# Kernel optimization log

Hardware: AMD Instinct MI355X
Metric: run time of the kernel (lower is better)

## Reference

```python
import jax, jax.numpy as jnp
import numpy as np

SOFT_BLEND = 20.0
INIT_BONES = np.array([0, 1, 2, 4, 5, 16, 17, 18, 19])
MAX_STEPS = 20
CVG_THRESH = 1e-5
DVG_THRESH = 1.0
EPS = 1e-6


def mlp(x, W0, b0, W1, b1, W2, b2):
    h = jax.nn.softplus(x @ W0 + b0)
    h = jax.nn.softplus(h @ W1 + b1)
    return h @ W2 + b2


def query_weights(x, params):
    # lbs_network -> soft_blend * logits -> softmax  (softmax_mode='softmax')
    return jax.nn.softmax(SOFT_BLEND * mlp(x, *params), axis=-1)


def forward_skinning(xc, params, tfs):
    # xc [B,N,3], tfs [B,J,4,4] -> xd [B,N,3]  (LBS: blend transforms with weights)
    w = query_weights(xc, params)                                    # [B,N,J]
    xh = jnp.concatenate([xc, jnp.ones_like(xc[..., :1])], -1)       # [B,N,4]
    return jnp.einsum('bpn,bnij,bpj->bpi', w, tfs, xh)[..., :3]


def gradient(xc, params, tfs):
    # per-point jacobian d(forward_skinning)/d(xc): [B,N,3,3]
    def f(x, tfs_b):
        w = query_weights(x, params)                                 # [J]
        xh = jnp.concatenate([x, jnp.ones((1,), x.dtype)])
        return jnp.einsum('j,jik,k->i', w, tfs_b, xh)[:3]
    jac = jax.jacfwd(f)
    return jax.vmap(jax.vmap(jac, in_axes=(0, None)), in_axes=(0, 0))(xc, tfs)


def broyden(g, x_init, J_inv_init):
    # vectorized Broyden: the torch data-dependent boolean masking becomes
    # mask-gated jnp.where updates; the early break becomes a fixed-length scan
    # (iterations are no-ops once ids_val is all False).
    x = x_init                                                       # [M,3,1]
    J_inv = J_inv_init                                               # [M,3,3]
    gx = g(x)
    update = -(J_inv @ gx)
    gx_norm_opt = jnp.linalg.norm(gx[..., 0], axis=-1)               # [M]
    state = (x, gx, J_inv, update, gx_norm_opt,
             jnp.zeros_like(x), jnp.zeros_like(gx),
             jnp.ones_like(gx_norm_opt, dtype=bool))

    def step(s, _):
        x, gx, J_inv, update, gx_norm_opt, delta_x, delta_gx, ids_val = s
        m = ids_val[:, None, None]
        delta_x = jnp.where(m, update, delta_x)
        x = x + jnp.where(m, delta_x, 0.0)
        gx_new = g(x)
        delta_gx = jnp.where(m, gx_new - gx, delta_gx)
        gx = jnp.where(m, gx_new, gx)
        gx_norm = jnp.linalg.norm(gx[..., 0], axis=-1)
        ids_opt = gx_norm < gx_norm_opt
        gx_norm_opt = jnp.where(ids_opt, gx_norm, gx_norm_opt)
        ids_val = (gx_norm_opt > CVG_THRESH) & (gx_norm < DVG_THRESH)
        m2 = ids_val[:, None, None]
        vT = jnp.swapaxes(delta_x, -1, -2) @ J_inv                   # [M,1,3]
        a = delta_x - J_inv @ delta_gx                               # [M,3,1]
        b = vT @ delta_gx                                            # [M,1,1]
        b = b + jnp.where(b >= 0, EPS, -EPS)
        J_inv = J_inv + jnp.where(m2, (a / b) @ vT, 0.0)
        update = -(J_inv @ gx)
        return (x, gx, J_inv, update, gx_norm_opt, delta_x, delta_gx, ids_val), None

    state, _ = jax.lax.scan(step, state, None, length=MAX_STEPS)
    # in the torch code x_opt aliases x, so the returned root is the final x
    return state[0], state[4]


def _forward(xd, tfs, W0, b0, W1, b1, W2, b2):
    params = (W0, b0, W1, b1, W2, b2)
    sg = jax.lax.stop_gradient
    B, N, D = xd.shape
    I = len(INIT_BONES)
    # ---- init: inverse rigid transform per init bone (one-hot weights) ----
    xdh = jnp.concatenate([xd, jnp.ones_like(xd[..., :1])], -1)      # [B,N,4]
    T_inv = jnp.linalg.inv(tfs[:, INIT_BONES])                        # [B,I,4,4]
    xc_init = jnp.einsum('bcij,bnj->bnci', T_inv, xdh)[..., :3]       # [B,N,I,3]
    # ---- Broyden correspondence search (torch.no_grad) ----
    params_sg = tuple(sg(p) for p in params)
    tfs_sg = sg(tfs)
    xc_flat = sg(xc_init).reshape(B, N * I, D)
    xd_tgt = sg(jnp.repeat(xd, I, axis=1))                            # [B,N*I,3]
    J_inv_init = jnp.linalg.inv(gradient(xc_flat, params_sg, tfs_sg)).reshape(-1, D, D)

    def g(x):                                                         # [M,3,1] -> [M,3,1]
        xc = x[..., 0].reshape(B, N * I, D)
        err = forward_skinning(xc, params_sg, tfs_sg) - xd_tgt
        return err.reshape(-1, D, 1)

    x_opt, _ = broyden(g, xc_flat.reshape(-1, D, 1), J_inv_init)
    xc_opt = sg(x_opt[..., 0].reshape(B, N * I, D))
    # ---- implicit differentiation correction term ----
    xd_opt = forward_skinning(xc_opt, params, tfs)
    grad_inv = sg(jnp.linalg.inv(gradient(xc_opt, params, tfs)))      # [B,M,3,3]
    correction = xd_opt - sg(xd_opt)
    correction = jnp.einsum('bnij,bnj->bni', -grad_inv, correction)
    return (xc_opt + correction).reshape(B, N, I, D)


def setup_inputs():
    key = jax.random.key(0)
    ks = jax.random.split(key, 6)
    B, N, J, W = 1, 30000, 24, 64
    xd = 0.5 * jax.random.normal(ks[0], (B, N, 3), jnp.float32)
    # near-rigid bone transforms: identity + small perturbation, homogeneous last row
    R = jnp.eye(3, dtype=jnp.float32) + 0.1 * jax.random.normal(ks[1], (B, J, 3, 3), jnp.float32)
    t = 0.2 * jax.random.normal(ks[2], (B, J, 3, 1), jnp.float32)
    bot = jnp.broadcast_to(jnp.array([0., 0., 0., 1.], jnp.float32), (B, J, 1, 4))
    tfs = jnp.concatenate([jnp.concatenate([R, t], -1), bot], -2)     # [B,J,4,4]
    W0 = 0.5 * jax.random.normal(ks[3], (3, W), jnp.float32)
    W1 = jax.random.normal(ks[4], (W, W), jnp.float32) / float(np.sqrt(W))
    W2 = 0.1 * jax.random.normal(ks[5], (W, J), jnp.float32) / float(np.sqrt(W))
    return {"xd": xd, "tfs": tfs,
            "W0": W0, "b0": jnp.zeros((W,), jnp.float32),
            "W1": W1, "b1": jnp.zeros((W,), jnp.float32),
            "W2": W2, "b2": jnp.zeros((J,), jnp.float32)}


def reference(xd, tfs, W0, b0, W1, b1, W2, b2):
    return _forward(xd, tfs, W0, b0, W1, b1, W2, b2)
```

## Files before the change

### kernel.cpp

```cpp
#include <hip/hip_runtime.h>
#include <math.h>

#define TPB 64
#define NPT 270000
#define SOFTB 20.0f
#define CVGT 1e-5f
#define DVGT 1.0f
#define EPSB 1e-6f

#define WS_TINV 0
#define WS_W0T  256

typedef __attribute__((ext_vector_type(2))) float f2;

__device__ __forceinline__ f2 pk_fma(f2 a, f2 b, f2 c) {
#if __has_builtin(__builtin_elementwise_fma)
    return __builtin_elementwise_fma(a, b, c);
#else
    f2 r; r.x = fmaf(a.x, b.x, c.x); r.y = fmaf(a.y, b.y, c.y); return r;
#endif
}

__global__ void prep_kernel(const float* __restrict__ tfs,
                            const float* __restrict__ W0, const float* __restrict__ b0,
                            float* __restrict__ ws) {
    int t = threadIdx.x;
    if (t < 9) {
        const int bones[9] = {0, 1, 2, 4, 5, 16, 17, 18, 19};
        const float* T = tfs + bones[t] * 16;
        float r00=T[0], r01=T[1], r02=T[2],  t0=T[3];
        float r10=T[4], r11=T[5], r12=T[6],  t1=T[7];
        float r20=T[8], r21=T[9], r22=T[10], t2=T[11];
        float c00 = r11*r22 - r12*r21;
        float c01 = r12*r20 - r10*r22;
        float c02 = r10*r21 - r11*r20;
        float det = r00*c00 + r01*c01 + r02*c02;
        float id  = 1.0f / det;
        float i00=c00*id, i01=(r02*r21-r01*r22)*id, i02=(r01*r12-r02*r11)*id;
        float i10=c01*id, i11=(r00*r22-r02*r20)*id, i12=(r02*r10-r00*r12)*id;
        float i20=c02*id, i21=(r01*r20-r00*r21)*id, i22=(r00*r11-r01*r10)*id;
        float* O = ws + WS_TINV + t * 16;
        O[0]=i00; O[1]=i01; O[2]=i02;  O[3]=-(i00*t0+i01*t1+i02*t2);
        O[4]=i10; O[5]=i11; O[6]=i12;  O[7]=-(i10*t0+i11*t1+i12*t2);
        O[8]=i20; O[9]=i21; O[10]=i22; O[11]=-(i20*t0+i21*t1+i22*t2);
        O[12]=0.f; O[13]=0.f; O[14]=0.f; O[15]=1.f;
    }
    for (int i = t; i < 64*4; i += 256) {
        int k = i >> 2, cidx = i & 3;
        ws[WS_W0T + i] = (cidx < 3) ? W0[cidx*64 + k] : b0[k];
    }
}

__global__ __launch_bounds__(TPB) void deform_kernel(
    const float* __restrict__ xd,
    const float* __restrict__ tfs,
    const float* __restrict__ W1, const float* __restrict__ b1,
    const float* __restrict__ W2, const float* __restrict__ b2,
    const float* __restrict__ ws,
    float* __restrict__ out)
{
    __shared__ float stash[24 * TPB];

    const int tid = threadIdx.x;
    const int p   = blockIdx.x * TPB + tid;
    const bool live = (p < NPT);
    const int pc = live ? p : 0;
    const int n  = pc / 9;
    const int c  = pc - n * 9;

    float tx0 = xd[n*3+0], tx1 = xd[n*3+1], tx2 = xd[n*3+2];

    const float* Ti  = ws + WS_TINV + c * 16;
    const float* W0T = ws + WS_W0T;

    float x0 = fmaf(Ti[0], tx0, fmaf(Ti[1], tx1, fmaf(Ti[2],  tx2, Ti[3])));
    float x1 = fmaf(Ti[4], tx0, fmaf(Ti[5], tx1, fmaf(Ti[6],  tx2, Ti[7])));
    float x2 = fmaf(Ti[8], tx0, fmaf(Ti[9], tx1, fmaf(Ti[10], tx2, Ti[11])));

    f2 wr[12];

    auto forward = [&](float a0, float a1, float a2, float& o0, float& o1, float& o2) {
        const f2* b2v = (const f2*)b2;
        #pragma unroll
        for (int q = 0; q < 12; ++q) wr[q] = b2v[q];
        #pragma unroll 1
        for (int cc = 0; cc < 2; ++cc) {
            f2 z1[16];
            const f2* b1c = (const f2*)(b1 + cc*32);
            #pragma unroll
            for (int j = 0; j < 16; ++j) z1[j] = b1c[j];
            #pragma unroll 2
            for (int k = 0; k < 64; ++k) {
                float w0a = W0T[k*4+0], w0b = W0T[k*4+1], w0c = W0T[k*4+2], w0d = W0T[k*4+3];
                float z  = fmaf(a0, w0a, fmaf(a1, w0b, fmaf(a2, w0c, w0d)));
                float hk = fmaxf(z, 0.f) + __logf(1.f + __expf(-fabsf(z)));
                f2 hk2 = hk;
                const f2* Wr2 = (const f2*)(W1 + k*64 + cc*32);
                #pragma unroll
                for (int j = 0; j < 16; ++j) z1[j] = pk_fma(hk2, Wr2[j], z1[j]);
            }
            #pragma unroll
            for (int j = 0; j < 16; ++j) {
                float za = z1[j].x, zb = z1[j].y;
                float ha = fmaxf(za, 0.f) + __logf(1.f + __expf(-fabsf(za)));
                float hb = fmaxf(zb, 0.f) + __logf(1.f + __expf(-fabsf(zb)));
                const f2* Wa = (const f2*)(W2 + (cc*32 + 2*j  )*24);
                const f2* Wb = (const f2*)(W2 + (cc*32 + 2*j+1)*24);
                f2 ha2 = ha, hb2 = hb;
                #pragma unroll
                for (int q = 0; q < 12; ++q) wr[q] = pk_fma(ha2, Wa[q], wr[q]);
                #pragma unroll
                for (int q = 0; q < 12; ++q) wr[q] = pk_fma(hb2, Wb[q], wr[q]);
            }
        }
        f2 m0 = __builtin_elementwise_max(wr[0], wr[1]);
        f2 m1 = __builtin_elementwise_max(wr[2], wr[3]);
        f2 m2 = __builtin_elementwise_max(wr[4], wr[5]);
        f2 m3 = __builtin_elementwise_max(wr[6], wr[7]);
        f2 m4 = __builtin_elementwise_max(wr[8], wr[9]);
        f2 m5 = __builtin_elementwise_max(wr[10], wr[11]);
        m0 = __builtin_elementwise_max(m0, m1);
        m2 = __builtin_elementwise_max(m2, m3);
        m4 = __builtin_elementwise_max(m4, m5);
        m0 = __builtin_elementwise_max(m0, m2);
        m0 = __builtin_elementwise_max(m0, m4);
        float mx = fmaxf(m0.x, m0.y);
        float ssum = 0.f;
        #pragma unroll
        for (int q = 0; q < 12; ++q) {
            float ea = __expf(SOFTB*(wr[q].x - mx));
            float eb = __expf(SOFTB*(wr[q].y - mx));
            wr[q].x = ea; wr[q].y = eb;
            ssum += ea; ssum += eb;
        }
        float inv = 1.0f / ssum;
        o0 = 0.f; o1 = 0.f; o2 = 0.f;
        #pragma unroll
        for (int q = 0; q < 24; ++q) {
            float wq = ((q & 1) ? wr[q>>1].y : wr[q>>1].x) * inv;
            if (q & 1) wr[q>>1].y = wq; else wr[q>>1].x = wq;
            const float* Tn = tfs + q*16;
            float y0 = fmaf(Tn[0], a0, fmaf(Tn[1], a1, fmaf(Tn[2],  a2, Tn[3])));
            float y1 = fmaf(Tn[4], a0, fmaf(Tn[5], a1, fmaf(Tn[6],  a2, Tn[7])));
            float y2 = fmaf(Tn[8], a0, fmaf(Tn[9], a1, fmaf(Tn[10], a2, Tn[11])));
            o0 = fmaf(wq, y0, o0); o1 = fmaf(wq, y1, o1); o2 = fmaf(wq, y2, o2);
        }
    };

    float f0, f1, f2s;
    forward(x0, x1, x2, f0, f1, f2s);

    #pragma unroll
    for (int q = 0; q < 24; ++q)
        stash[q*TPB + tid] = (q & 1) ? wr[q>>1].y : wr[q>>1].x;

    float Jm[9];
    #pragma unroll 1
    for (int t = 0; t < 3; ++t) {
        float dot = 0.f, sA = 0.f, sB = 0.f, sC = 0.f;
        #pragma unroll 1
        for (int cc = 0; cc < 4; ++cc) {
            f2 z1c[8], d1c[8];
            const f2* b1c = (const f2*)(b1 + cc*16);
            #pragma unroll
            for (int j = 0; j < 8; ++j) { z1c[j] = b1c[j]; d1c[j] = (f2)0.f; }
            #pragma unroll 2
            for (int k = 0; k < 64; ++k) {
                float w0a = W0T[k*4+0], w0b = W0T[k*4+1], w0c = W0T[k*4+2], w0d = W0T[k*4+3];
                float wt  = W0T[k*4 + t];
                float z  = fmaf(x0, w0a, fmaf(x1, w0b, fmaf(x2, w0c, w0d)));
                float e  = __expf(-z);
                float hk = z + __logf(1.f + e);
                float sg = 1.0f / (1.0f + e);
                float dh0 = sg * wt;
                f2 hk2 = hk, dh02 = dh0;
                const f2* Wr2 = (const f2*)(W1 + k*64 + cc*16);
                #pragma unroll
                for (int j = 0; j < 8; ++j) {
                    z1c[j] = pk_fma(hk2,  Wr2[j], z1c[j]);
                    d1c[j] = pk_fma(dh02, Wr2[j], d1c[j]);
                }
            }
            f2 dmc[12];
            #pragma unroll
            for (int q = 0; q < 12; ++q) dmc[q] = (f2)0.f;
            #pragma unroll
            for (int j = 0; j < 16; ++j) {
                float zz = (j & 1) ? z1c[j>>1].y : z1c[j>>1].x;
                float dd = (j & 1) ? d1c[j>>1].y : d1c[j>>1].x;
                float sg1 = 1.0f / (1.0f + __expf(-zz));
                float dh1 = dd * sg1;
                f2 dh12 = dh1;
                const f2* W2r = (const f2*)(W2 + (cc*16 + j)*24);
                #pragma unroll
                for (int q = 0; q < 12; ++q) dmc[q] = pk_fma(dh12, W2r[q], dmc[q]);
            }
            #pragma unroll
            for (int q = 0; q < 24; ++q) {
                float dmq = (q & 1) ? dmc[q>>1].y : dmc[q>>1].x;
                float wd = stash[q*TPB + tid] * dmq;
                dot += wd;
                const float* Tn = tfs + q*16;
                float y0 = fmaf(Tn[0], x0, fmaf(Tn[1], x1, fmaf(Tn[2],  x2, Tn[3])));
                float y1 = fmaf(Tn[4], x0, fmaf(Tn[5], x1, fmaf(Tn[6],  x2, Tn[7])));
                float y2 = fmaf(Tn[8], x0, fmaf(Tn[9], x1, fmaf(Tn[10], x2, Tn[11])));
                sA = fmaf(wd, y0, sA); sB = fmaf(wd, y1, sB); sC = fmaf(wd, y2, sC);
            }
        }
        float ab0 = 0.f, ab1 = 0.f, ab2 = 0.f;
        #pragma unroll
        for (int q = 0; q < 24; ++q) {
            float wq = stash[q*TPB + tid];
            const float* Tn = tfs + q*16;
            ab0 = fmaf(wq, Tn[0 + t], ab0);
            ab1 = fmaf(wq, Tn[4 + t], ab1);
            ab2 = fmaf(wq, Tn[8 + t], ab2);
        }
        Jm[0 + t] = ab0 + SOFTB*(sA - dot*f0);
        Jm[3 + t] = ab1 + SOFTB*(sB - dot*f1);
        Jm[6 + t] = ab2 + SOFTB*(sC - dot*f2s);
    }

    {
        float m00=Jm[0], m01=Jm[1], m02=Jm[2];
        float m10=Jm[3], m11=Jm[4], m12=Jm[5];
        float m20=Jm[6], m21=Jm[7], m22=Jm[8];
        float c00 = m11*m22 - m12*m21, c01 = m12*m20 - m10*m22, c02 = m10*m21 - m11*m20;
        float det = m00*c00 + m01*c01 + m02*c02;
        float idet = 1.0f / det;
        stash[ 0*TPB+tid] = c00*idet;
        stash[ 1*TPB+tid] = (m02*m21-m01*m22)*idet;
        stash[ 2*TPB+tid] = (m01*m12-m02*m11)*idet;
        stash[ 3*TPB+tid] = c01*idet;
        stash[ 4*TPB+tid] = (m00*m22-m02*m20)*idet;
        stash[ 5*TPB+tid] = (m02*m10-m00*m12)*idet;
        stash[ 6*TPB+tid] = c02*idet;
        stash[ 7*TPB+tid] = (m01*m20-m00*m21)*idet;
        stash[ 8*TPB+tid] = (m00*m11-m01*m10)*idet;
    }
    stash[13*TPB+tid] = tx0;
    stash[14*TPB+tid] = tx1;
    stash[15*TPB+tid] = tx2;

    float g0 = f0 - tx0, g1 = f1 - tx1, g2 = f2s - tx2;
    float u0, u1, u2;
    {
        float Ji0=stash[0*TPB+tid], Ji1=stash[1*TPB+tid], Ji2=stash[2*TPB+tid];
        float Ji3=stash[3*TPB+tid], Ji4=stash[4*TPB+tid], Ji5=stash[5*TPB+tid];
        float Ji6=stash[6*TPB+tid], Ji7=stash[7*TPB+tid], Ji8=stash[8*TPB+tid];
        stash[9*TPB+tid] = sqrtf(g0*g0 + g1*g1 + g2*g2);
        u0 = -(Ji0*g0 + Ji1*g1 + Ji2*g2);
        u1 = -(Ji3*g0 + Ji4*g1 + Ji5*g2);
        u2 = -(Ji6*g0 + Ji7*g1 + Ji8*g2);
    }
    bool valid = true;

    for (int it = 0; it < 20; ++it) {
        if (!__any((int)valid)) break;
        if (valid) {
            stash[10*TPB+tid] = u0;
            stash[11*TPB+tid] = u1;
            stash[12*TPB+tid] = u2;
            x0 += u0; x1 += u1; x2 += u2;
            float fn0, fn1, fn2;
            forward(x0, x1, x2, fn0, fn1, fn2);
            float ng0 = fn0 - stash[13*TPB+tid];
            float ng1 = fn1 - stash[14*TPB+tid];
            float ng2 = fn2 - stash[15*TPB+tid];
            float dg0 = ng0 - g0, dg1 = ng1 - g1, dg2 = ng2 - g2;
            g0 = ng0; g1 = ng1; g2 = ng2;
            float gn  = sqrtf(g0*g0 + g1*g1 + g2*g2);
            float gno = fminf(gn, stash[9*TPB+tid]);
            stash[9*TPB+tid] = gno;
            valid = (gno > CVGT) && (gn < DVGT);
            if (valid) {
                float Ji0=stash[0*TPB+tid], Ji1=stash[1*TPB+tid], Ji2=stash[2*TPB+tid];
                float Ji3=stash[3*TPB+tid], Ji4=stash[4*TPB+tid], Ji5=stash[5*TPB+tid];
                float Ji6=stash[6*TPB+tid], Ji7=stash[7*TPB+tid], Ji8=stash[8*TPB+tid];
                float dx0=stash[10*TPB+tid], dx1=stash[11*TPB+tid], dx2=stash[12*TPB+tid];
                float v0 = dx0*Ji0 + dx1*Ji3 + dx2*Ji6;
                float v1 = dx0*Ji1 + dx1*Ji4 + dx2*Ji7;
                float v2 = dx0*Ji2 + dx1*Ji5 + dx2*Ji8;
                float a0 = dx0 - (Ji0*dg0 + Ji1*dg1 + Ji2*dg2);
                float a1 = dx1 - (Ji3*dg0 + Ji4*dg1 + Ji5*dg2);
                float a2 = dx2 - (Ji6*dg0 + Ji7*dg1 + Ji8*dg2);
                float b = v0*dg0 + v1*dg1 + v2*dg2;
                b += (b >= 0.f) ? EPSB : -EPSB;
                float ib = 1.0f / b;
                a0 *= ib; a1 *= ib; a2 *= ib;
                Ji0 = fmaf(a0, v0, Ji0); Ji1 = fmaf(a0, v1, Ji1); Ji2 = fmaf(a0, v2, Ji2);
                Ji3 = fmaf(a1, v0, Ji3); Ji4 = fmaf(a1, v1, Ji4); Ji5 = fmaf(a1, v2, Ji5);
                Ji6 = fmaf(a2, v0, Ji6); Ji7 = fmaf(a2, v1, Ji7); Ji8 = fmaf(a2, v2, Ji8);
                stash[0*TPB+tid]=Ji0; stash[1*TPB+tid]=Ji1; stash[2*TPB+tid]=Ji2;
                stash[3*TPB+tid]=Ji3; stash[4*TPB+tid]=Ji4; stash[5*TPB+tid]=Ji5;
                stash[6*TPB+tid]=Ji6; stash[7*TPB+tid]=Ji7; stash[8*TPB+tid]=Ji8;
                u0 = -(Ji0*g0 + Ji1*g1 + Ji2*g2);
                u1 = -(Ji3*g0 + Ji4*g1 + Ji5*g2);
                u2 = -(Ji6*g0 + Ji7*g1 + Ji8*g2);
            }
        }
    }

    if (live) {
        out[p*3+0] = x0;
        out[p*3+1] = x1;
        out[p*3+2] = x2;
    }
}

extern "C" void kernel_launch(void* const* d_in, const int* in_sizes, int n_in,
                              void* d_out, int out_size, void* d_ws, size_t ws_size,
                              hipStream_t stream) {
    const float* xd  = (const float*)d_in[0];
    const float* tfs = (const float*)d_in[1];
    const float* W0  = (const float*)d_in[2];
    const float* b0  = (const float*)d_in[3];
    const float* W1  = (const float*)d_in[4];
    const float* b1  = (const float*)d_in[5];
    const float* W2  = (const float*)d_in[6];
    const float* b2  = (const float*)d_in[7];
    float* out = (float*)d_out;
    float* ws  = (float*)d_ws;

    prep_kernel<<<1, 256, 0, stream>>>(tfs, W0, b0, ws);
    int nblk = (NPT + TPB - 1) / TPB;
    deform_kernel<<<nblk, TPB, 0, stream>>>(xd, tfs, W1, b1, W2, b2, ws, out);
}
```

Before: 798.4 us.

## Compute all three Jacobian columns in one pass over the MLP hidden layer

The Jacobian used to be built one input column at a time, and each pass recomputed the layer-0 softplus and the layer-1 pre-activations. It now runs a single loop over eight chunks of eight hidden units and carries three tangent accumulators (dA, dB, dC) beside z1, which cuts the repeated exp/log and W1 fma work roughly threefold. The diff also swaps exact divisions for the fast reciprocal intrinsic. The price is more live registers per thread, which could reduce occupancy or cause spills.

```diff
diff --git a/kernel.cpp b/kernel.cpp
--- a/kernel.cpp
+++ b/kernel.cpp
@@ -154,44 +154,52 @@
     for (int q = 0; q < 24; ++q)
         stash[q*TPB + tid] = (q & 1) ? wr[q>>1].y : wr[q>>1].x;
 
-    float Jm[9];
+    float dt0=0.f, dt1=0.f, dt2=0.f;
+    float sx0=0.f, sx1=0.f, sx2=0.f;
+    float sy0=0.f, sy1=0.f, sy2=0.f;
+    float sz0=0.f, sz1=0.f, sz2=0.f;
     #pragma unroll 1
-    for (int t = 0; t < 3; ++t) {
-        float dot = 0.f, sA = 0.f, sB = 0.f, sC = 0.f;
-        #pragma unroll 1
-        for (int cc = 0; cc < 4; ++cc) {
-            f2 z1c[8], d1c[8];
-            const f2* b1c = (const f2*)(b1 + cc*16);
-            #pragma unroll
-            for (int j = 0; j < 8; ++j) { z1c[j] = b1c[j]; d1c[j] = (f2)0.f; }
-            #pragma unroll 2
-            for (int k = 0; k < 64; ++k) {
-                float w0a = W0T[k*4+0], w0b = W0T[k*4+1], w0c = W0T[k*4+2], w0d = W0T[k*4+3];
-                float wt  = W0T[k*4 + t];
-                float z  = fmaf(x0, w0a, fmaf(x1, w0b, fmaf(x2, w0c, w0d)));
-                float e  = __expf(-z);
-                float hk = z + __logf(1.f + e);
-                float sg = 1.0f / (1.0f + e);
-                float dh0 = sg * wt;
-                f2 hk2 = hk, dh02 = dh0;
-                const f2* Wr2 = (const f2*)(W1 + k*64 + cc*16);
-                #pragma unroll
-                for (int j = 0; j < 8; ++j) {
-                    z1c[j] = pk_fma(hk2,  Wr2[j], z1c[j]);
-                    d1c[j] = pk_fma(dh02, Wr2[j], d1c[j]);
-                }
-            }
+    for (int cc = 0; cc < 8; ++cc) {
+        f2 z1c[4], dA[4], dB[4], dC[4];
+        const f2* b1c = (const f2*)(b1 + cc*8);
+        #pragma unroll
+        for (int j = 0; j < 4; ++j) {
+            z1c[j] = b1c[j]; dA[j] = (f2)0.f; dB[j] = (f2)0.f; dC[j] = (f2)0.f;
+        }
+        #pragma unroll 2
+        for (int k = 0; k < 64; ++k) {
+            float w0a = W0T[k*4+0], w0b = W0T[k*4+1], w0c = W0T[k*4+2], w0d = W0T[k*4+3];
+            float z  = fmaf(x0, w0a, fmaf(x1, w0b, fmaf(x2, w0c, w0d)));
+            float e  = __expf(-z);
+            float hk = z + __logf(1.f + e);
+            float sg = __builtin_amdgcn_rcpf(1.f + e);
+            float da = sg * w0a, db = sg * w0b, dc = sg * w0c;
+            f2 hk2 = hk, da2 = da, db2 = db, dc2 = dc;
+            const f2* Wr2 = (const f2*)(W1 + k*64 + cc*8);
+            #pragma unroll
+            for (int j = 0; j < 4; ++j) {
+                z1c[j] = pk_fma(hk2, Wr2[j], z1c[j]);
+                dA[j]  = pk_fma(da2, Wr2[j], dA[j]);
+                dB[j]  = pk_fma(db2, Wr2[j], dB[j]);
+                dC[j]  = pk_fma(dc2, Wr2[j], dC[j]);
+            }
+        }
+        float sg1[8];
+        #pragma unroll
+        for (int j = 0; j < 8; ++j) {
+            float zz = (j & 1) ? z1c[j>>1].y : z1c[j>>1].x;
+            sg1[j] = __builtin_amdgcn_rcpf(1.f + __expf(-zz));
+        }
+        auto do_t = [&](const f2* dX, float& dt, float& sx, float& sy, float& sz) {
             f2 dmc[12];
             #pragma unroll
             for (int q = 0; q < 12; ++q) dmc[q] = (f2)0.f;
             #pragma unroll
-            for (int j = 0; j < 16; ++j) {
-                float zz = (j & 1) ? z1c[j>>1].y : z1c[j>>1].x;
-                float dd = (j & 1) ? d1c[j>>1].y : d1c[j>>1].x;
-                float sg1 = 1.0f / (1.0f + __expf(-zz));
-                float dh1 = dd * sg1;
+            for (int j = 0; j < 8; ++j) {
+                float dd  = (j & 1) ? dX[j>>1].y : dX[j>>1].x;
+                float dh1 = dd * sg1[j];
                 f2 dh12 = dh1;
-                const f2* W2r = (const f2*)(W2 + (cc*16 + j)*24);
+                const f2* W2r = (const f2*)(W2 + (cc*8 + j)*24);
                 #pragma unroll
                 for (int q = 0; q < 12; ++q) dmc[q] = pk_fma(dh12, W2r[q], dmc[q]);
             }
@@ -199,32 +207,41 @@
             for (int q = 0; q < 24; ++q) {
                 float dmq = (q & 1) ? dmc[q>>1].y : dmc[q>>1].x;
                 float wd = stash[q*TPB + tid] * dmq;
-                dot += wd;
+                dt += wd;
                 const float* Tn = tfs + q*16;
                 float y0 = fmaf(Tn[0], x0, fmaf(Tn[1], x1, fmaf(Tn[2],  x2, Tn[3])));
                 float y1 = fmaf(Tn[4], x0, fmaf(Tn[5], x1, fmaf(Tn[6],  x2, Tn[7])));
                 float y2 = fmaf(Tn[8], x0, fmaf(Tn[9], x1, fmaf(Tn[10], x2, Tn[11])));
-                sA = fmaf(wd, y0, sA); sB = fmaf(wd, y1, sB); sC = fmaf(wd, y2, sC);
-            }
-        }
-        float ab0 = 0.f, ab1 = 0.f, ab2 = 0.f;
-        #pragma unroll
-        for (int q = 0; q < 24; ++q) {
-            float wq = stash[q*TPB + tid];
-            const float* Tn = tfs + q*16;
-            ab0 = fmaf(wq, Tn[0 + t], ab0);
-            ab1 = fmaf(wq, Tn[4 + t], ab1);
-            ab2 = fmaf(wq, Tn[8 + t], ab2);
-        }
-        Jm[0 + t] = ab0 + SOFTB*(sA - dot*f0);
-        Jm[3 + t] = ab1 + SOFTB*(sB - dot*f1);
-        Jm[6 + t] = ab2 + SOFTB*(sC - dot*f2s);
-    }
+                sx = fmaf(wd, y0, sx); sy = fmaf(wd, y1, sy); sz = fmaf(wd, y2, sz);
+            }
+        };
+        do_t(dA, dt0, sx0, sy0, sz0);
+        do_t(dB, dt1, sx1, sy1, sz1);
+        do_t(dC, dt2, sx2, sy2, sz2);
+    }
+
+    float ab00=0.f, ab01=0.f, ab02=0.f;
+    float ab10=0.f, ab11=0.f, ab12=0.f;
+    float ab20=0.f, ab21=0.f, ab22=0.f;
+    #pragma unroll
+    for (int q = 0; q < 24; ++q) {
+        float wq = stash[q*TPB + tid];
+        const float* Tn = tfs + q*16;
+        ab00 = fmaf(wq, Tn[0],  ab00); ab01 = fmaf(wq, Tn[1],  ab01); ab02 = fmaf(wq, Tn[2],  ab02);
+        ab10 = fmaf(wq, Tn[4],  ab10); ab11 = fmaf(wq, Tn[5],  ab11); ab12 = fmaf(wq, Tn[6],  ab12);
+        ab20 = fmaf(wq, Tn[8],  ab20); ab21 = fmaf(wq, Tn[9],  ab21); ab22 = fmaf(wq, Tn[10], ab22);
+    }
+    float m00 = ab00 + SOFTB*(sx0 - dt0*f0);
+    float m01 = ab01 + SOFTB*(sx1 - dt1*f0);
+    float m02 = ab02 + SOFTB*(sx2 - dt2*f0);
+    float m10 = ab10 + SOFTB*(sy0 - dt0*f1);
+    float m11 = ab11 + SOFTB*(sy1 - dt1*f1);
+    float m12 = ab12 + SOFTB*(sy2 - dt2*f1);
+    float m20 = ab20 + SOFTB*(sz0 - dt0*f2s);
+    float m21 = ab21 + SOFTB*(sz1 - dt1*f2s);
+    float m22 = ab22 + SOFTB*(sz2 - dt2*f2s);
 
     {
-        float m00=Jm[0], m01=Jm[1], m02=Jm[2];
-        float m10=Jm[3], m11=Jm[4], m12=Jm[5];
-        float m20=Jm[6], m21=Jm[7], m22=Jm[8];
         float c00 = m11*m22 - m12*m21, c01 = m12*m20 - m10*m22, c02 = m10*m21 - m11*m20;
         float det = m00*c00 + m01*c01 + m02*c02;
         float idet = 1.0f / det;
```

Measured after the change: 1.135 ms. 1.42x slower.

## Split each point across two threads by halving hidden layer-2 units

Applied to the files above, without the earlier changes.

Each point is now handled by a pair of adjacent lanes. Each lane computes half of the second hidden layer's units and its share of the output logits and jacobian contributions, then the pair combines partial sums with xor-shuffles. The launch uses twice as many threads, and only the even lane writes the result. This aims to cut per-thread serial FMA work and raise parallelism. In exchange, both lanes repeat the layer-1 softplus, the softmax, the bone transforms and the Broyden bookkeeping, and the change adds shuffle traffic.

```diff
diff --git a/kernel.cpp b/kernel.cpp
--- a/kernel.cpp
+++ b/kernel.cpp
@@ -62,7 +62,9 @@
     __shared__ float stash[24 * TPB];
 
     const int tid = threadIdx.x;
-    const int p   = blockIdx.x * TPB + tid;
+    const int gt  = blockIdx.x * TPB + tid;
+    const int p    = gt >> 1;
+    const int half = gt & 1;
     const bool live = (p < NPT);
     const int pc = live ? p : 0;
     const int n  = pc / 9;
@@ -82,36 +84,40 @@
     auto forward = [&](float a0, float a1, float a2, float& o0, float& o1, float& o2) {
         const f2* b2v = (const f2*)b2;
         #pragma unroll
-        for (int q = 0; q < 12; ++q) wr[q] = b2v[q];
-        #pragma unroll 1
-        for (int cc = 0; cc < 2; ++cc) {
-            f2 z1[16];
-            const f2* b1c = (const f2*)(b1 + cc*32);
-            #pragma unroll
-            for (int j = 0; j < 16; ++j) z1[j] = b1c[j];
-            #pragma unroll 2
-            for (int k = 0; k < 64; ++k) {
-                float w0a = W0T[k*4+0], w0b = W0T[k*4+1], w0c = W0T[k*4+2], w0d = W0T[k*4+3];
-                float z  = fmaf(a0, w0a, fmaf(a1, w0b, fmaf(a2, w0c, w0d)));
-                float hk = fmaxf(z, 0.f) + __logf(1.f + __expf(-fabsf(z)));
-                f2 hk2 = hk;
-                const f2* Wr2 = (const f2*)(W1 + k*64 + cc*32);
-                #pragma unroll
-                for (int j = 0; j < 16; ++j) z1[j] = pk_fma(hk2, Wr2[j], z1[j]);
-            }
-            #pragma unroll
-            for (int j = 0; j < 16; ++j) {
-                float za = z1[j].x, zb = z1[j].y;
-                float ha = fmaxf(za, 0.f) + __logf(1.f + __expf(-fabsf(za)));
-                float hb = fmaxf(zb, 0.f) + __logf(1.f + __expf(-fabsf(zb)));
-                const f2* Wa = (const f2*)(W2 + (cc*32 + 2*j  )*24);
-                const f2* Wb = (const f2*)(W2 + (cc*32 + 2*j+1)*24);
-                f2 ha2 = ha, hb2 = hb;
-                #pragma unroll
-                for (int q = 0; q < 12; ++q) wr[q] = pk_fma(ha2, Wa[q], wr[q]);
-                #pragma unroll
-                for (int q = 0; q < 12; ++q) wr[q] = pk_fma(hb2, Wb[q], wr[q]);
-            }
+        for (int q = 0; q < 12; ++q) wr[q] = half ? (f2)0.f : b2v[q];
+        f2 z1[16];
+        const f2* b1v = (const f2*)(b1 + half*32);
+        #pragma unroll
+        for (int j = 0; j < 16; ++j) z1[j] = b1v[j];
+        #pragma unroll 2
+        for (int k = 0; k < 64; ++k) {
+            float w0a = W0T[k*4+0], w0b = W0T[k*4+1], w0c = W0T[k*4+2], w0d = W0T[k*4+3];
+            float z  = fmaf(a0, w0a, fmaf(a1, w0b, fmaf(a2, w0c, w0d)));
+            float hk = fmaxf(z, 0.f) + __logf(1.f + __expf(-fabsf(z)));
+            f2 hk2 = hk;
+            const f2* Wr2 = (const f2*)(W1 + k*64 + half*32);
+            #pragma unroll
+            for (int j = 0; j < 16; ++j) z1[j] = pk_fma(hk2, Wr2[j], z1[j]);
+        }
+        #pragma unroll
+        for (int j = 0; j < 16; ++j) {
+            float za = z1[j].x, zb = z1[j].y;
+            float ha = fmaxf(za, 0.f) + __logf(1.f + __expf(-fabsf(za)));
+            float hb = fmaxf(zb, 0.f) + __logf(1.f + __expf(-fabsf(zb)));
+            const f2* Wa = (const f2*)(W2 + (half*32 + 2*j  )*24);
+            const f2* Wb = (const f2*)(W2 + (half*32 + 2*j+1)*24);
+            f2 ha2 = ha, hb2 = hb;
+            #pragma unroll
+            for (int q = 0; q < 12; ++q) wr[q] = pk_fma(ha2, Wa[q], wr[q]);
+            #pragma unroll
+            for (int q = 0; q < 12; ++q) wr[q] = pk_fma(hb2, Wb[q], wr[q]);
+        }
+        #pragma unroll
+        for (int q = 0; q < 12; ++q) {
+            f2 o;
+            o.x = __shfl_xor(wr[q].x, 1, 64);
+            o.y = __shfl_xor(wr[q].y, 1, 64);
+            wr[q] += o;
         }
         f2 m0 = __builtin_elementwise_max(wr[0], wr[1]);
         f2 m1 = __builtin_elementwise_max(wr[2], wr[3]);
@@ -159,9 +165,9 @@
     for (int t = 0; t < 3; ++t) {
         float dot = 0.f, sA = 0.f, sB = 0.f, sC = 0.f;
         #pragma unroll 1
-        for (int cc = 0; cc < 4; ++cc) {
+        for (int cc = 0; cc < 2; ++cc) {
             f2 z1c[8], d1c[8];
-            const f2* b1c = (const f2*)(b1 + cc*16);
+            const f2* b1c = (const f2*)(b1 + half*32 + cc*16);
             #pragma unroll
             for (int j = 0; j < 8; ++j) { z1c[j] = b1c[j]; d1c[j] = (f2)0.f; }
             #pragma unroll 2
@@ -174,7 +180,7 @@
                 float sg = 1.0f / (1.0f + e);
                 float dh0 = sg * wt;
                 f2 hk2 = hk, dh02 = dh0;
-                const f2* Wr2 = (const f2*)(W1 + k*64 + cc*16);
+                const f2* Wr2 = (const f2*)(W1 + k*64 + half*32 + cc*16);
                 #pragma unroll
                 for (int j = 0; j < 8; ++j) {
                     z1c[j] = pk_fma(hk2,  Wr2[j], z1c[j]);
@@ -191,9 +197,16 @@
                 float sg1 = 1.0f / (1.0f + __expf(-zz));
                 float dh1 = dd * sg1;
                 f2 dh12 = dh1;
-                const f2* W2r = (const f2*)(W2 + (cc*16 + j)*24);
+                const f2* W2r = (const f2*)(W2 + (half*32 + cc*16 + j)*24);
                 #pragma unroll
                 for (int q = 0; q < 12; ++q) dmc[q] = pk_fma(dh12, W2r[q], dmc[q]);
+            }
+            #pragma unroll
+            for (int q = 0; q < 12; ++q) {
+                f2 o;
+                o.x = __shfl_xor(dmc[q].x, 1, 64);
+                o.y = __shfl_xor(dmc[q].y, 1, 64);
+                dmc[q] += o;
             }
             #pragma unroll
             for (int q = 0; q < 24; ++q) {
@@ -301,7 +314,7 @@
         }
     }
 
-    if (live) {
+    if (live && half == 0) {
         out[p*3+0] = x0;
         out[p*3+1] = x1;
         out[p*3+2] = x2;
@@ -323,6 +336,6 @@
     float* ws  = (float*)d_ws;
 
     prep_kernel<<<1, 256, 0, stream>>>(tfs, W0, b0, ws);
-    int nblk = (NPT + TPB - 1) / TPB;
+    int nblk = (2*NPT + TPB - 1) / TPB;
     deform_kernel<<<nblk, TPB, 0, stream>>>(xd, tfs, W1, b1, W2, b2, ws, out);
 }
```

Measured after the change: 2.368 ms. 2.97x slower.
